# Kernel optimization log

Measured on AMD Instinct MI355X. Metric: run time of the kernel, lower is better.

## Reference

```python
import jax, jax.numpy as jnp
import numpy as np


def conv3x3(x, w, b):
    # stride 1, pad 1, NCHW / OIHW
    out = jax.lax.conv_general_dilated(x, w, (1, 1), ((1, 1), (1, 1)),
                                       dimension_numbers=('NCHW', 'OIHW', 'NCHW'))
    return out + b[None, :, None, None]


def bilinear_sample(x, ys, xs):
    # x: [B,C,H,W]; ys,xs: [B,K,H,W] float sampling coords.
    # mmcv-style: zero outside image, per-corner validity.
    B, C, H, W = x.shape
    x_flat = x.reshape(B, C, H * W)
    y0 = jnp.floor(ys)
    x0 = jnp.floor(xs)
    dy = ys - y0
    dx = xs - x0
    y0i = y0.astype(jnp.int32)
    x0i = x0.astype(jnp.int32)

    def corner(yc, xc, wgt):
        valid = (yc >= 0) & (yc < H) & (xc >= 0) & (xc < W)
        idx = jnp.clip(yc, 0, H - 1) * W + jnp.clip(xc, 0, W - 1)  # [B,K,H,W]
        idx_f = idx.reshape(B, -1)
        vals = jax.vmap(lambda xf, ix: xf[:, ix])(x_flat, idx_f)  # [B,C,K*H*W]
        vals = vals.reshape(B, C, *yc.shape[1:])
        return vals * (wgt * valid)[:, None]

    out = corner(y0i, x0i, (1 - dy) * (1 - dx))
    out = out + corner(y0i, x0i + 1, (1 - dy) * dx)
    out = out + corner(y0i + 1, x0i, dy * (1 - dx))
    out = out + corner(y0i + 1, x0i + 1, dy * dx)
    return out  # [B,C,K,H,W]


def avgpool3s2(z):
    # AvgPool2d(kernel=3, stride=2, padding=1), count_include_pad=True -> divide by 9
    s = jax.lax.reduce_window(z, 0.0, jax.lax.add, (1, 1, 3, 3), (1, 1, 2, 2),
                              ((0, 0), (0, 0), (1, 1), (1, 1)))
    return s / 9.0


def setup_inputs() -> dict:
    key = jax.random.key(0)
    k1, k2, k3 = jax.random.split(key, 3)
    C = 64
    x = jax.random.normal(k1, (4, C, 128, 128), dtype=jnp.float32)
    w_off = jax.random.normal(k2, (27, C, 3, 3), dtype=jnp.float32) * 0.02
    b_off = jnp.zeros((27,), dtype=jnp.float32)
    w_align = jax.random.normal(k3, (C, C, 3, 3), dtype=jnp.float32) * 0.02
    b_align = jnp.zeros((C,), dtype=jnp.float32)
    return {"x": x, "w_off": w_off, "b_off": b_off, "w_align": w_align, "b_align": b_align}


def reference(x, w_off, b_off, w_align, b_align):
    B, C, H, W = x.shape
    K = 9
    off_all = conv3x3(x, w_off, b_off)               # [B,27,H,W]
    offset = off_all[:, :2 * K]                      # [B,18,H,W]
    mask = 2.0 * jax.nn.sigmoid(off_all[:, 2 * K:])  # [B,9,H,W]
    off = offset.reshape(B, K, 2, H, W)
    dy = off[:, :, 0]
    dx = off[:, :, 1]
    # base kernel grid (dilation 1, pad 1): offsets in {-1,0,1}
    ky = (jnp.arange(K) // 3 - 1).astype(jnp.float32)
    kx = (jnp.arange(K) % 3 - 1).astype(jnp.float32)
    ys = jnp.arange(H, dtype=jnp.float32)[None, None, :, None] + ky[None, :, None, None] + dy
    xs = jnp.arange(W, dtype=jnp.float32)[None, None, None, :] + kx[None, :, None, None] + dx
    sampled = bilinear_sample(x, ys, xs) * mask[:, None]    # [B,C,K,H,W]
    w = jnp.einsum('bckhw,ock->bohw', sampled, w_align.reshape(C, C, K))
    w = w + b_align[None, :, None, None]
    w = jnp.exp(jax.nn.sigmoid(w))
    return avgpool3s2(w * x) / avgpool3s2(w)
```

## Files before the change

kernel.cpp:

```cpp
#include <hip/hip_runtime.h>
#include <hip/hip_bf16.h>

#define HW 16384
#define CC 64
#define BB 4

typedef __attribute__((ext_vector_type(8))) short bf8;
typedef __attribute__((ext_vector_type(4))) float f4;

static __device__ __forceinline__ float bf2f(unsigned short u) {
    return __uint_as_float(((unsigned)u) << 16);
}
static __device__ __forceinline__ unsigned short f2bf(float f) {
    __hip_bfloat16 h = __float2bfloat16(f);
    return *reinterpret_cast<unsigned short*>(&h);
}

__global__ __launch_bounds__(256) void k_prep_tx(const float* __restrict__ x,
                                                 const float* __restrict__ w_off,
                                                 const float* __restrict__ w_align,
                                                 unsigned short* __restrict__ xT,
                                                 unsigned short* __restrict__ wA2,
                                                 unsigned short* __restrict__ Wal2) {
    __shared__ unsigned T32[64 * 33];
    int bx = blockIdx.x, t = threadIdx.x;
    if (bx < 216) {
        int i = bx * 256 + t;
        if (i < 32 * 576) {
            int jj = i & 7;
            int chunk = i >> 3;
            int l = chunk & 63;
            int g = chunk >> 6;
            int m2 = g & 1;
            int h2 = (g >> 1) & 1;
            int tp = g >> 2;
            int m = m2 * 16 + (l & 15);
            int c = h2 * 32 + (l >> 4) * 8 + jj;
            float v = (m < 27) ? w_off[m * 576 + c * 9 + tp] : 0.f;
            wA2[i] = f2bf(v);
        } else {
            int j = i - 32 * 576;
            int jj = j & 7;
            int chunk = j >> 3;
            int l = chunk & 63;
            int g = chunk >> 6;
            int mt = g & 3;
            int th = g >> 2;
            int h2 = th & 1;
            int tp = th >> 1;
            int o = mt * 16 + (l & 15);
            int c = h2 * 32 + (l >> 4) * 8 + jj;
            Wal2[j] = f2bf(w_align[o * 576 + c * 9 + tp]);
        }
        return;
    }
    int pix0 = (bx - 216) * 64;
    int b = pix0 >> 14, hw0 = pix0 & (HW - 1);
    const float* xb = x + (size_t)b * CC * HW + hw0;
#pragma unroll
    for (int u = 0; u < 8; u++) {
        int i = t + 256 * u;
        int cp = i >> 6, p = i & 63;
        float v0 = xb[(size_t)(2 * cp) * HW + p];
        float v1 = xb[(size_t)(2 * cp + 1) * HW + p];
        T32[p * 33 + cp] = (unsigned)f2bf(v0) | ((unsigned)f2bf(v1) << 16);
    }
    __syncthreads();
#pragma unroll
    for (int u = 0; u < 2; u++) {
        int i = t + 256 * u;
        int p = i >> 3, q = i & 7;
        uint4 qq;
        qq.x = T32[p * 33 + q * 4 + 0];
        qq.y = T32[p * 33 + q * 4 + 1];
        qq.z = T32[p * 33 + q * 4 + 2];
        qq.w = T32[p * 33 + q * 4 + 3];
        *(uint4*)(xT + ((size_t)b * HW + hw0 + p) * CC + q * 8) = qq;
    }
}

__global__ __launch_bounds__(256, 4) void k_conv(const unsigned short* __restrict__ xT,
                                                 const unsigned short* __restrict__ wA2,
                                                 const float* __restrict__ b_off,
                                                 float* __restrict__ off) {
    __shared__ __align__(16) unsigned short TC[198 * 64];
    int t = threadIdx.x, lane = t & 63, wv = t >> 6;
    int quad = lane >> 4, col = lane & 15;
    int n0 = blockIdx.x * 64;
    int b = n0 >> 14, hw0 = n0 & (HW - 1);
    int h = hw0 >> 7, w0 = hw0 & 127;
    int pxo = wv * 16 + col;
    int hw = hw0 + pxo, w = w0 + pxo;
    const unsigned short* xTb = xT + (size_t)b * HW * CC;

#pragma unroll
    for (int u = 0; u < 7; u++) {
        int i = t + 256 * u;
        if (i < 1584) {
            int e = i >> 3, s = i & 7;
            int ty = e / 66, tx = e - ty * 66;
            int gy = min(max(h - 1 + ty, 0), 127);
            int gx = min(max(w0 - 1 + tx, 0), 127);
            int c = s ^ (e & 7);
            uint4 q = *(const uint4*)(xTb + ((size_t)((gy << 7) + gx)) * CC + c * 8);
            *(uint4*)(TC + i * 8) = q;
        }
    }
    __syncthreads();

    const bf8 zero = {0, 0, 0, 0, 0, 0, 0, 0};
    f4 acc0 = {0.f, 0.f, 0.f, 0.f};
    f4 acc1 = {0.f, 0.f, 0.f, 0.f};
#pragma unroll
    for (int tap = 0; tap < 9; tap++) {
        int dyt = tap / 3 - 1, dxt = tap - (tap / 3) * 3 - 1;
        int hs = h + dyt, ws = w + dxt;
        bool valid = ((unsigned)hs < 128u) && ((unsigned)ws < 128u);
        int e = (dyt + 1) * 66 + pxo + dxt + 1;
        int sL = quad ^ (e & 7);
        bf8 b0 = *(const bf8*)(TC + e * 64 + (sL << 3));
        bf8 b1 = *(const bf8*)(TC + e * 64 + ((sL ^ 4) << 3));
        b0 = valid ? b0 : zero;
        b1 = valid ? b1 : zero;
        const bf8 a00 = *(const bf8*)(wA2 + (((tap * 4 + 0) * 64 + lane) << 3));
        const bf8 a01 = *(const bf8*)(wA2 + (((tap * 4 + 1) * 64 + lane) << 3));
        const bf8 a10 = *(const bf8*)(wA2 + (((tap * 4 + 2) * 64 + lane) << 3));
        const bf8 a11 = *(const bf8*)(wA2 + (((tap * 4 + 3) * 64 + lane) << 3));
        acc0 = __builtin_amdgcn_mfma_f32_16x16x32_bf16(a00, b0, acc0, 0, 0, 0);
        acc1 = __builtin_amdgcn_mfma_f32_16x16x32_bf16(a01, b0, acc1, 0, 0, 0);
        acc0 = __builtin_amdgcn_mfma_f32_16x16x32_bf16(a10, b1, acc0, 0, 0, 0);
        acc1 = __builtin_amdgcn_mfma_f32_16x16x32_bf16(a11, b1, acc1, 0, 0, 0);
    }
#pragma unroll
    for (int i = 0; i < 4; i++) {
        int o0 = quad * 4 + i;
        {
            float v = acc0[i] + b_off[o0];
            if (o0 >= 18) v = 2.f / (1.f + __expf(-v));
            off[((size_t)b * 27 + o0) * HW + hw] = v;
        }
        int o1 = 16 + o0;
        if (o1 < 27) {
            float v = acc1[i] + b_off[o1];
            if (o1 >= 18) v = 2.f / (1.f + __expf(-v));
            off[((size_t)b * 27 + o1) * HW + hw] = v;
        }
    }
}

__global__ __launch_bounds__(256, 3) void k_fused(const unsigned short* __restrict__ xT,
                                                  const float* __restrict__ off,
                                                  const unsigned short* __restrict__ Wal2,
                                                  const float* __restrict__ b_align,
                                                  float* __restrict__ wten) {
    __shared__ __align__(16) unsigned short TF[420 * 64];

    int t = threadIdx.x, lane = t & 63, wv = t >> 6;
    int quad = lane >> 4, col = lane & 15;
    int pix0 = blockIdx.x * 64;
    int b = pix0 >> 14, hw0 = pix0 & (HW - 1);
    int h = hw0 >> 7, w0 = hw0 & 127;
    int pxo = wv * 16 + col;
    int px = hw0 + pxo, w = w0 + pxo;
    const unsigned short* xTb = xT + (size_t)b * HW * CC;
    const float* offp = off + (size_t)b * 27 * HW + px;
    const unsigned short* wl = Wal2 + lane * 8;

    float dyv[9], dxv[9], mv[9];
#pragma unroll
    for (int k = 0; k < 9; k++) {
        dyv[k] = offp[(size_t)(2 * k) * HW];
        dxv[k] = offp[(size_t)(2 * k + 1) * HW];
        mv[k]  = offp[(size_t)(18 + k) * HW];
    }

#pragma unroll
    for (int u = 0; u < 14; u++) {
        int i = t + 256 * u;
        if (i < 3360) {
            int e = i >> 3, s = i & 7;
            int ty = e / 70, tx = e - ty * 70;
            int gy = min(max(h - 2 + ty, 0), 127);
            int gx = min(max(w0 - 3 + tx, 0), 127);
            int c = s ^ (e & 7);
            uint4 q = *(const uint4*)(xTb + ((size_t)((gy << 7) + gx)) * CC + c * 8);
            *(uint4*)(TF + i * 8) = q;
        }
    }
    __syncthreads();

    int hm2 = h - 2, hp3 = h + 3, wm3 = w0 - 3, wp66 = w0 + 66;

    f4 acc[4];
#pragma unroll
    for (int mt = 0; mt < 4; mt++) acc[mt] = (f4){0.f, 0.f, 0.f, 0.f};

#pragma unroll
    for (int k = 0; k < 9; k++) {
        float dy = dyv[k], dx = dxv[k], m = mv[k];
        int k3 = k / 3;
        float ys = (float)(h + k3 - 1) + dy;
        float xs = (float)(w + (k - 3 * k3) - 1) + dx;
        float y0f = floorf(ys), x0f = floorf(xs);
        float fy = ys - y0f, fx = xs - x0f;
        int y0 = (int)y0f, x0 = (int)x0f;
        int y1 = y0 + 1, x1 = x0 + 1;
        bool vy0 = (unsigned)y0 < 128u, vy1 = (unsigned)y1 < 128u;
        bool vx0 = (unsigned)x0 < 128u, vx1 = (unsigned)x1 < 128u;
        int cy0 = min(max(y0, 0), 127), cy1 = min(max(y1, 0), 127);
        int cx0 = min(max(x0, 0), 127), cx1 = min(max(x1, 0), 127);
        float w00 = (1.f - fy) * (1.f - fx) * ((vy0 && vx0) ? m : 0.f);
        float w01 = (1.f - fy) * fx         * ((vy0 && vx1) ? m : 0.f);
        float w10 = fy * (1.f - fx)         * ((vy1 && vx0) ? m : 0.f);
        float w11 = fy * fx                 * ((vy1 && vx1) ? m : 0.f);

        bool inT = (cy0 >= hm2) & (cy1 <= hp3) & (cx0 >= wm3) & (cx1 <= wp66);
        uint4 qa0, qa1, qa2, qa3, qb0, qb1, qb2, qb3;
        if (inT) {
            int r0 = (cy0 - hm2) * 70 - wm3, r1 = (cy1 - hm2) * 70 - wm3;
            int e00 = r0 + cx0, e01 = r0 + cx1, e10 = r1 + cx0, e11 = r1 + cx1;
            int s00 = quad ^ (e00 & 7), s01 = quad ^ (e01 & 7);
            int s10 = quad ^ (e10 & 7), s11 = quad ^ (e11 & 7);
            qa0 = *(const uint4*)(TF + e00 * 64 + (s00 << 3));
            qa1 = *(const uint4*)(TF + e01 * 64 + (s01 << 3));
            qa2 = *(const uint4*)(TF + e10 * 64 + (s10 << 3));
            qa3 = *(const uint4*)(TF + e11 * 64 + (s11 << 3));
            qb0 = *(const uint4*)(TF + e00 * 64 + ((s00 ^ 4) << 3));
            qb1 = *(const uint4*)(TF + e01 * 64 + ((s01 ^ 4) << 3));
            qb2 = *(const uint4*)(TF + e10 * 64 + ((s10 ^ 4) << 3));
            qb3 = *(const uint4*)(TF + e11 * 64 + ((s11 ^ 4) << 3));
        } else {
            const unsigned short* c00 = xTb + ((size_t)(cy0 * 128 + cx0)) * CC + quad * 8;
            const unsigned short* c01 = xTb + ((size_t)(cy0 * 128 + cx1)) * CC + quad * 8;
            const unsigned short* c10 = xTb + ((size_t)(cy1 * 128 + cx0)) * CC + quad * 8;
            const unsigned short* c11 = xTb + ((size_t)(cy1 * 128 + cx1)) * CC + quad * 8;
            qa0 = *(const uint4*)(c00);      qa1 = *(const uint4*)(c01);
            qa2 = *(const uint4*)(c10);      qa3 = *(const uint4*)(c11);
            qb0 = *(const uint4*)(c00 + 32); qb1 = *(const uint4*)(c01 + 32);
            qb2 = *(const uint4*)(c10 + 32); qb3 = *(const uint4*)(c11 + 32);
        }

        bf8 bfrag[2];
#pragma unroll
        for (int h2 = 0; h2 < 2; h2++) {
            const unsigned short* u00 = (const unsigned short*)(h2 ? &qb0 : &qa0);
            const unsigned short* u01 = (const unsigned short*)(h2 ? &qb1 : &qa1);
            const unsigned short* u10 = (const unsigned short*)(h2 ? &qb2 : &qa2);
            const unsigned short* u11 = (const unsigned short*)(h2 ? &qb3 : &qa3);
            unsigned short ov[8];
#pragma unroll
            for (int j = 0; j < 8; j++) {
                float v = w00 * bf2f(u00[j]) + w01 * bf2f(u01[j])
                        + w10 * bf2f(u10[j]) + w11 * bf2f(u11[j]);
                ov[j] = f2bf(v);
            }
            bfrag[h2] = *(const bf8*)ov;
        }
#pragma unroll
        for (int h2 = 0; h2 < 2; h2++) {
#pragma unroll
            for (int mt = 0; mt < 4; mt++) {
                const bf8 a = *(const bf8*)(wl + (size_t)(((k * 2 + h2) * 4 + mt) * 512));
                acc[mt] = __builtin_amdgcn_mfma_f32_16x16x32_bf16(a, bfrag[h2], acc[mt], 0, 0, 0);
            }
        }
    }

    float* wb = wten + (size_t)b * CC * HW + px;
#pragma unroll
    for (int mt = 0; mt < 4; mt++)
#pragma unroll
        for (int i = 0; i < 4; i++) {
            int o = mt * 16 + quad * 4 + i;
            float u = acc[mt][i] + b_align[o];
            float sg = 1.f / (1.f + __expf(-u));
            wb[(size_t)o * HW] = __expf(sg);
        }
}

__global__ __launch_bounds__(256) void k_pool(const float* __restrict__ x,
                                              const float* __restrict__ wten,
                                              float* __restrict__ out) {
    int idx = blockIdx.x * 256 + threadIdx.x;
    int ow = idx & 63;
    int oh = (idx >> 6) & 63;
    int bc = idx >> 12;
    const float* wp = wten + (size_t)bc * HW;
    const float* xp = x + (size_t)bc * HW;
    float num = 0.f, den = 0.f;
#pragma unroll
    for (int iy = 0; iy < 3; iy++) {
        int y = 2 * oh + iy - 1;
        if ((unsigned)y >= 128u) continue;
#pragma unroll
        for (int ix = 0; ix < 3; ix++) {
            int xc = 2 * ow + ix - 1;
            if ((unsigned)xc >= 128u) continue;
            float wv = wp[y * 128 + xc];
            float xv = xp[y * 128 + xc];
            num = fmaf(wv, xv, num);
            den += wv;
        }
    }
    out[idx] = num / den;
}

extern "C" void kernel_launch(void* const* d_in, const int* in_sizes, int n_in,
                              void* d_out, int out_size, void* d_ws, size_t ws_size,
                              hipStream_t stream) {
    const float* x       = (const float*)d_in[0];
    const float* w_off   = (const float*)d_in[1];
    const float* b_off   = (const float*)d_in[2];
    const float* w_align = (const float*)d_in[3];
    const float* b_align = (const float*)d_in[4];
    float* out = (float*)d_out;

    char* p = (char*)d_ws;
    float* off  = (float*)p;                  p += (size_t)BB * 27 * HW * 4;
    float* wten = (float*)p;                  p += (size_t)BB * CC * HW * 4;
    unsigned short* xT  = (unsigned short*)p; p += (size_t)BB * HW * CC * 2;
    unsigned short* wA2 = (unsigned short*)p; p += 32 * 576 * 2;
    unsigned short* Wal2 = (unsigned short*)p;

    k_prep_tx<<<dim3(1240), dim3(256), 0, stream>>>(x, w_off, w_align, xT, wA2, Wal2);
    k_conv<<<dim3(1024), dim3(256), 0, stream>>>(xT, wA2, b_off, off);
    k_fused<<<dim3(1024), dim3(256), 0, stream>>>(xT, off, Wal2, b_align, wten);
    k_pool<<<dim3(4096), dim3(256), 0, stream>>>(x, wten, out);
}
```

Measured before the change: 117.0 us.

## Fuse offset/mask conv into deformable sampling kernel via shared tile

Removes the separate offset convolution kernel and computes the 27-channel offset/mask conv inside the fused deformable kernel, reusing the already-staged x tile in LDS and passing results through a small shared buffer. The tile is shrunk from 6 to 5 rows, which cuts LDS use and load work but sends more bilinear taps to the global fallback path. This eliminates one launch and the global write and read of the offset tensor, at the cost of extra MFMA work and an extra barrier in the fused kernel.

```diff
diff --git a/kernel.cpp b/kernel.cpp
--- a/kernel.cpp
+++ b/kernel.cpp
@@ -79,81 +79,14 @@
     }
 }
 
-__global__ __launch_bounds__(256, 4) void k_conv(const unsigned short* __restrict__ xT,
-                                                 const unsigned short* __restrict__ wA2,
-                                                 const float* __restrict__ b_off,
-                                                 float* __restrict__ off) {
-    __shared__ __align__(16) unsigned short TC[198 * 64];
-    int t = threadIdx.x, lane = t & 63, wv = t >> 6;
-    int quad = lane >> 4, col = lane & 15;
-    int n0 = blockIdx.x * 64;
-    int b = n0 >> 14, hw0 = n0 & (HW - 1);
-    int h = hw0 >> 7, w0 = hw0 & 127;
-    int pxo = wv * 16 + col;
-    int hw = hw0 + pxo, w = w0 + pxo;
-    const unsigned short* xTb = xT + (size_t)b * HW * CC;
-
-#pragma unroll
-    for (int u = 0; u < 7; u++) {
-        int i = t + 256 * u;
-        if (i < 1584) {
-            int e = i >> 3, s = i & 7;
-            int ty = e / 66, tx = e - ty * 66;
-            int gy = min(max(h - 1 + ty, 0), 127);
-            int gx = min(max(w0 - 1 + tx, 0), 127);
-            int c = s ^ (e & 7);
-            uint4 q = *(const uint4*)(xTb + ((size_t)((gy << 7) + gx)) * CC + c * 8);
-            *(uint4*)(TC + i * 8) = q;
-        }
-    }
-    __syncthreads();
-
-    const bf8 zero = {0, 0, 0, 0, 0, 0, 0, 0};
-    f4 acc0 = {0.f, 0.f, 0.f, 0.f};
-    f4 acc1 = {0.f, 0.f, 0.f, 0.f};
-#pragma unroll
-    for (int tap = 0; tap < 9; tap++) {
-        int dyt = tap / 3 - 1, dxt = tap - (tap / 3) * 3 - 1;
-        int hs = h + dyt, ws = w + dxt;
-        bool valid = ((unsigned)hs < 128u) && ((unsigned)ws < 128u);
-        int e = (dyt + 1) * 66 + pxo + dxt + 1;
-        int sL = quad ^ (e & 7);
-        bf8 b0 = *(const bf8*)(TC + e * 64 + (sL << 3));
-        bf8 b1 = *(const bf8*)(TC + e * 64 + ((sL ^ 4) << 3));
-        b0 = valid ? b0 : zero;
-        b1 = valid ? b1 : zero;
-        const bf8 a00 = *(const bf8*)(wA2 + (((tap * 4 + 0) * 64 + lane) << 3));
-        const bf8 a01 = *(const bf8*)(wA2 + (((tap * 4 + 1) * 64 + lane) << 3));
-        const bf8 a10 = *(const bf8*)(wA2 + (((tap * 4 + 2) * 64 + lane) << 3));
-        const bf8 a11 = *(const bf8*)(wA2 + (((tap * 4 + 3) * 64 + lane) << 3));
-        acc0 = __builtin_amdgcn_mfma_f32_16x16x32_bf16(a00, b0, acc0, 0, 0, 0);
-        acc1 = __builtin_amdgcn_mfma_f32_16x16x32_bf16(a01, b0, acc1, 0, 0, 0);
-        acc0 = __builtin_amdgcn_mfma_f32_16x16x32_bf16(a10, b1, acc0, 0, 0, 0);
-        acc1 = __builtin_amdgcn_mfma_f32_16x16x32_bf16(a11, b1, acc1, 0, 0, 0);
-    }
-#pragma unroll
-    for (int i = 0; i < 4; i++) {
-        int o0 = quad * 4 + i;
-        {
-            float v = acc0[i] + b_off[o0];
-            if (o0 >= 18) v = 2.f / (1.f + __expf(-v));
-            off[((size_t)b * 27 + o0) * HW + hw] = v;
-        }
-        int o1 = 16 + o0;
-        if (o1 < 27) {
-            float v = acc1[i] + b_off[o1];
-            if (o1 >= 18) v = 2.f / (1.f + __expf(-v));
-            off[((size_t)b * 27 + o1) * HW + hw] = v;
-        }
-    }
-}
-
 __global__ __launch_bounds__(256, 3) void k_fused(const unsigned short* __restrict__ xT,
-                                                  const float* __restrict__ off,
+                                                  const unsigned short* __restrict__ wA2,
                                                   const unsigned short* __restrict__ Wal2,
+                                                  const float* __restrict__ b_off,
                                                   const float* __restrict__ b_align,
                                                   float* __restrict__ wten) {
-    __shared__ __align__(16) unsigned short TF[420 * 64];
+    __shared__ __align__(16) unsigned short TF[350 * 64];
+    __shared__ float OB[27 * 65];
 
     int t = threadIdx.x, lane = t & 63, wv = t >> 6;
     int quad = lane >> 4, col = lane & 15;
@@ -163,21 +96,12 @@
     int pxo = wv * 16 + col;
     int px = hw0 + pxo, w = w0 + pxo;
     const unsigned short* xTb = xT + (size_t)b * HW * CC;
-    const float* offp = off + (size_t)b * 27 * HW + px;
     const unsigned short* wl = Wal2 + lane * 8;
 
-    float dyv[9], dxv[9], mv[9];
-#pragma unroll
-    for (int k = 0; k < 9; k++) {
-        dyv[k] = offp[(size_t)(2 * k) * HW];
-        dxv[k] = offp[(size_t)(2 * k + 1) * HW];
-        mv[k]  = offp[(size_t)(18 + k) * HW];
-    }
-
-#pragma unroll
-    for (int u = 0; u < 14; u++) {
+#pragma unroll
+    for (int u = 0; u < 11; u++) {
         int i = t + 256 * u;
-        if (i < 3360) {
+        if (i < 2800) {
             int e = i >> 3, s = i & 7;
             int ty = e / 70, tx = e - ty * 70;
             int gy = min(max(h - 2 + ty, 0), 127);
@@ -189,7 +113,53 @@
     }
     __syncthreads();
 
-    int hm2 = h - 2, hp3 = h + 3, wm3 = w0 - 3, wp66 = w0 + 66;
+    {
+        const bf8 zero = {0, 0, 0, 0, 0, 0, 0, 0};
+        f4 a0 = {0.f, 0.f, 0.f, 0.f};
+        f4 a1 = {0.f, 0.f, 0.f, 0.f};
+#pragma unroll
+        for (int tap = 0; tap < 9; tap++) {
+            int dyt = tap / 3 - 1, dxt = tap - (tap / 3) * 3 - 1;
+            int hs = h + dyt, ws = w + dxt;
+            bool valid = ((unsigned)hs < 128u) && ((unsigned)ws < 128u);
+            int e = (dyt + 2) * 70 + pxo + dxt + 3;
+            int sL = quad ^ (e & 7);
+            bf8 b0 = *(const bf8*)(TF + e * 64 + (sL << 3));
+            bf8 b1 = *(const bf8*)(TF + e * 64 + ((sL ^ 4) << 3));
+            b0 = valid ? b0 : zero;
+            b1 = valid ? b1 : zero;
+            const bf8 a00 = *(const bf8*)(wA2 + (((tap * 4 + 0) * 64 + lane) << 3));
+            const bf8 a01 = *(const bf8*)(wA2 + (((tap * 4 + 1) * 64 + lane) << 3));
+            const bf8 a10 = *(const bf8*)(wA2 + (((tap * 4 + 2) * 64 + lane) << 3));
+            const bf8 a11 = *(const bf8*)(wA2 + (((tap * 4 + 3) * 64 + lane) << 3));
+            a0 = __builtin_amdgcn_mfma_f32_16x16x32_bf16(a00, b0, a0, 0, 0, 0);
+            a1 = __builtin_amdgcn_mfma_f32_16x16x32_bf16(a01, b0, a1, 0, 0, 0);
+            a0 = __builtin_amdgcn_mfma_f32_16x16x32_bf16(a10, b1, a0, 0, 0, 0);
+            a1 = __builtin_amdgcn_mfma_f32_16x16x32_bf16(a11, b1, a1, 0, 0, 0);
+        }
+#pragma unroll
+        for (int i = 0; i < 4; i++) {
+            int o0 = quad * 4 + i;
+            OB[o0 * 65 + pxo] = a0[i] + b_off[o0];
+            int o1 = 16 + o0;
+            if (o1 < 27) {
+                float v = a1[i] + b_off[o1];
+                if (o1 >= 18) v = 2.f / (1.f + __expf(-v));
+                OB[o1 * 65 + pxo] = v;
+            }
+        }
+    }
+    __syncthreads();
+
+    float dyv[9], dxv[9], mv[9];
+#pragma unroll
+    for (int k = 0; k < 9; k++) {
+        dyv[k] = OB[(2 * k) * 65 + pxo];
+        dxv[k] = OB[(2 * k + 1) * 65 + pxo];
+        mv[k]  = OB[(18 + k) * 65 + pxo];
+    }
+
+    int hm2 = h - 2, hp2 = h + 2, wm3 = w0 - 3, wp66 = w0 + 66;
 
     f4 acc[4];
 #pragma unroll
@@ -214,7 +184,7 @@
         float w10 = fy * (1.f - fx)         * ((vy1 && vx0) ? m : 0.f);
         float w11 = fy * fx                 * ((vy1 && vx1) ? m : 0.f);
 
-        bool inT = (cy0 >= hm2) & (cy1 <= hp3) & (cx0 >= wm3) & (cx1 <= wp66);
+        bool inT = (cy0 >= hm2) & (cy1 <= hp2) & (cx0 >= wm3) & (cx1 <= wp66);
         uint4 qa0, qa1, qa2, qa3, qb0, qb1, qb2, qb3;
         if (inT) {
             int r0 = (cy0 - hm2) * 70 - wm3, r1 = (cy1 - hm2) * 70 - wm3;
@@ -316,14 +286,12 @@
     float* out = (float*)d_out;
 
     char* p = (char*)d_ws;
-    float* off  = (float*)p;                  p += (size_t)BB * 27 * HW * 4;
     float* wten = (float*)p;                  p += (size_t)BB * CC * HW * 4;
     unsigned short* xT  = (unsigned short*)p; p += (size_t)BB * HW * CC * 2;
     unsigned short* wA2 = (unsigned short*)p; p += 32 * 576 * 2;
     unsigned short* Wal2 = (unsigned short*)p;
 
     k_prep_tx<<<dim3(1240), dim3(256), 0, stream>>>(x, w_off, w_align, xT, wA2, Wal2);
-    k_conv<<<dim3(1024), dim3(256), 0, stream>>>(xT, wA2, b_off, off);
-    k_fused<<<dim3(1024), dim3(256), 0, stream>>>(xT, off, Wal2, b_align, wten);
+    k_fused<<<dim3(1024), dim3(256), 0, stream>>>(xT, wA2, Wal2, b_off, b_align, wten);
     k_pool<<<dim3(4096), dim3(256), 0, stream>>>(x, wten, out);
 }
```

New measurement: 112.9 us. 3.6% less time.
